# Performance work log

Measured on AMD Instinct MI355X. Metric: run time of the kernel, lower is better.

## Reference

```python
import jax, jax.numpy as jnp
import numpy as np

H = 256  # hidden_dim


def _bidir_lstm_layer(x, W_ih, W_hh, bias):
    """x: [S, B, in]; W_ih: [2, in, 4H]; W_hh: [2, H, 4H]; bias: [2, 4H].
    Returns [S, B, 2H] (forward || backward outputs per timestep).
    PyTorch gate order: i, f, g, o."""
    B = x.shape[1]
    init = (jnp.zeros((B, H), x.dtype), jnp.zeros((B, H), x.dtype))
    # precompute input projections for the whole sequence, both directions
    xp = jnp.einsum('sbi,dij->dsbj', x, W_ih) + bias[:, None, None, :]  # [2,S,B,4H]

    def make_step(W_hh_d):
        def step(carry, xt):
            h, c = carry
            g = xt + h @ W_hh_d  # [B, 4H]
            i = jax.nn.sigmoid(g[:, :H])
            f = jax.nn.sigmoid(g[:, H:2 * H])
            gg = jnp.tanh(g[:, 2 * H:3 * H])
            o = jax.nn.sigmoid(g[:, 3 * H:])
            c = f * c + i * gg
            h = o * jnp.tanh(c)
            return (h, c), h
        return step

    _, h_f = jax.lax.scan(make_step(W_hh[0]), init, xp[0])
    _, h_b = jax.lax.scan(make_step(W_hh[1]), init, xp[1], reverse=True)
    return jnp.concatenate([h_f, h_b], axis=-1)  # [S, B, 2H]


def setup_inputs() -> dict:
    key = jax.random.key(0)
    ks = jax.random.split(key, 11)
    s = 0.05  # small init scale to keep gates in their dynamic range
    inp = {
        'x': jax.random.normal(ks[0], (8192, 1024), jnp.float32),
        'w_ih0': jax.random.normal(ks[1], (2, 1024, 4 * H), jnp.float32) * s,
        'w_hh0': jax.random.normal(ks[2], (2, H, 4 * H), jnp.float32) * s,
        'b0': jax.random.normal(ks[3], (2, 4 * H), jnp.float32) * s,
        'w_ih': jax.random.normal(ks[4], (4, 2, 2 * H, 4 * H), jnp.float32) * s,
        'w_hh': jax.random.normal(ks[5], (4, 2, H, 4 * H), jnp.float32) * s,
        'b': jax.random.normal(ks[6], (4, 2, 4 * H), jnp.float32) * s,
        'w1': jax.random.normal(ks[7], (2 * H, 32), jnp.float32) * s,
        'b1': jax.random.normal(ks[8], (32,), jnp.float32) * s,
        'w2': jax.random.normal(ks[9], (32, 2), jnp.float32) * s,
        'b2': jax.random.normal(ks[10], (2,), jnp.float32) * s,
    }
    return inp


def reference(x, w_ih0, w_hh0, b0, w_ih, w_hh, b, w1, b1, w2, b2):
    # x: [S, 1024] -> [S, B=1, 1024] (module does unsqueeze(0).transpose(0,1))
    h = x[:, None, :]
    h = _bidir_lstm_layer(h, w_ih0, w_hh0, b0)
    for l in range(4):  # layers 1..4 (fixed count)
        h = _bidir_lstm_layer(h, w_ih[l], w_hh[l], b[l])
    # cat(forward output at last step, backward output at first step)
    feat = jnp.concatenate([h[-1, :, :H], h[0, :, H:]], axis=1)  # [1, 2H]
    out = (feat @ w1 + b1) @ w2 + b2  # [1, 2]
    return out
```

## Files before the change

### kernel.cpp

```cpp
#include <hip/hip_runtime.h>

constexpr int SQ = 8192;
constexpr int HD = 256;
constexpr int NG = 1024;

typedef __fp16 h2 __attribute__((ext_vector_type(2)));
typedef unsigned int uint;

__device__ __forceinline__ float sigm_f(float x) {
  float e = __builtin_amdgcn_exp2f(-1.4426950408889634f * x);
  return __builtin_amdgcn_rcpf(1.0f + e);
}
__device__ __forceinline__ float tanh_f(float x) {
  float e = __builtin_amdgcn_exp2f(2.885390081777927f * x);
  return 1.0f - 2.0f * __builtin_amdgcn_rcpf(1.0f + e);
}
__device__ __forceinline__ h2 bch2(uint v) { return __builtin_bit_cast(h2, v); }
__device__ __forceinline__ uint pk(float a, float b) {
  return __builtin_bit_cast(uint, __builtin_amdgcn_cvt_pkrtz(a, b));
}

__global__ __launch_bounds__(256) void gemm_xp(const float* __restrict__ A, int K,
                                               const float* __restrict__ W,
                                               const float* __restrict__ bias,
                                               float* __restrict__ out) {
  __shared__ float Al[16][64];
  __shared__ float Bl[16][64];
  const int tid = threadIdx.x;
  const int bm = blockIdx.x * 64;
  const int d  = blockIdx.y >> 4;
  const int bn = (blockIdx.y & 15) * 64;
  const float* Wd = W + (size_t)d * K * NG;
  const float* bd = bias + (size_t)d * NG;
  float* outd = out + (size_t)d * SQ * NG;

  const int m4 = (tid >> 4) << 2;
  const int n4 = (tid & 15) << 2;
  const int am = tid >> 2, ak = (tid & 3) << 2;
  const int bk = tid >> 4, bnn = (tid & 15) << 2;

  float acc[4][4] = {};
  for (int kt = 0; kt < K; kt += 16) {
    float4 av = *(const float4*)(A + (size_t)(bm + am) * K + kt + ak);
    float4 bv = *(const float4*)(Wd + (size_t)(kt + bk) * NG + bn + bnn);
    __syncthreads();
    Al[ak + 0][am] = av.x;
    Al[ak + 1][am] = av.y;
    Al[ak + 2][am] = av.z;
    Al[ak + 3][am] = av.w;
    *(float4*)&Bl[bk][bnn] = bv;
    __syncthreads();
#pragma unroll
    for (int k = 0; k < 16; ++k) {
      float4 a = *(const float4*)&Al[k][m4];
      float4 b = *(const float4*)&Bl[k][n4];
      float ar[4] = {a.x, a.y, a.z, a.w};
      float br[4] = {b.x, b.y, b.z, b.w};
#pragma unroll
      for (int i = 0; i < 4; ++i)
#pragma unroll
        for (int jj = 0; jj < 4; ++jj)
          acc[i][jj] = fmaf(ar[i], br[jj], acc[i][jj]);
    }
  }
#pragma unroll
  for (int i = 0; i < 4; ++i) {
    float4 o;
    o.x = acc[i][0] + bd[bn + n4 + 0];
    o.y = acc[i][1] + bd[bn + n4 + 1];
    o.z = acc[i][2] + bd[bn + n4 + 2];
    o.w = acc[i][3] + bd[bn + n4 + 3];
    *(float4*)(outd + (size_t)(bm + m4 + i) * NG + bn + n4) = o;
  }
}

__global__ __launch_bounds__(512, 1) void lstm_rec4(const float* __restrict__ Whh,
                                                    const float* __restrict__ xp,
                                                    float* __restrict__ obuf) {
  __shared__ uint4 wl4[8 * 1024];
  __shared__ float glds[1024];
  __shared__ uint4 hlds[32];
  const int d = blockIdx.x;
  const int j = threadIdx.x;
  const int w = j >> 6;
  const int l = j & 63;
  const int li = l & 31;
  const int s  = l >> 5;
  const float* W   = Whh + (size_t)d * HD * NG;
  const float* xpd = xp + (size_t)d * SQ * NG;
  const int cbase = w * 128 + li;

  for (int idx = j; idx < 8 * 1024; idx += 512) {
    const int q8 = idx >> 10;
    const int c  = idx & 1023;
    const int ss = q8 >> 2, q = q8 & 3;
    const int r0 = ss * 128 + 96 + 8 * q;
    uint4 v;
    v.x = pk(W[(size_t)(r0 + 0) * NG + c], W[(size_t)(r0 + 1) * NG + c]);
    v.y = pk(W[(size_t)(r0 + 2) * NG + c], W[(size_t)(r0 + 3) * NG + c]);
    v.z = pk(W[(size_t)(r0 + 4) * NG + c], W[(size_t)(r0 + 5) * NG + c]);
    v.w = pk(W[(size_t)(r0 + 6) * NG + c], W[(size_t)(r0 + 7) * NG + c]);
    wl4[q8 * 1024 + c] = v;
  }

  h2 wr[4][48];
#pragma unroll
  for (int i = 0; i < 4; ++i) {
    const float* Wc = W + (size_t)(s * 128) * NG + cbase + 32 * i;
#pragma unroll
    for (int k = 0; k < 48; ++k)
      wr[i][k] = __builtin_amdgcn_cvt_pkrtz(Wc[(size_t)(2 * k) * NG],
                                            Wc[(size_t)(2 * k + 1) * NG]);
  }

  if (j < 32) hlds[j] = make_uint4(0u, 0u, 0u, 0u);
  __syncthreads();

  const int fwd = (d == 0) ? 1 : 0;
  int t = fwd ? 0 : SQ - 1;
  const int dt = fwd ? 1 : -1;
  float cc = 0.0f;

  float xc[4] = {}, xn[4] = {};
  if (s == 0) {
#pragma unroll
    for (int i = 0; i < 4; ++i) xc[i] = xpd[(size_t)t * NG + cbase + 32 * i];
  }

  for (int step = 0; step < SQ; ++step) {
    if (s == 0 && step + 1 < SQ) {
#pragma unroll
      for (int i = 0; i < 4; ++i) xn[i] = xpd[(size_t)(t + dt) * NG + cbase + 32 * i];
    }

    float acc[4] = {0.0f, 0.0f, 0.0f, 0.0f};
    const uint4* hb = hlds + s * 16;

#pragma unroll
    for (int q = 0; q < 12; ++q) {
      uint4 hq = hb[q];
      h2 hx = bch2(hq.x), hy = bch2(hq.y), hz = bch2(hq.z), hw = bch2(hq.w);
#pragma unroll
      for (int i = 0; i < 4; ++i) {
        acc[i] = __builtin_amdgcn_fdot2(wr[i][4 * q + 0], hx, acc[i], false);
        acc[i] = __builtin_amdgcn_fdot2(wr[i][4 * q + 1], hy, acc[i], false);
        acc[i] = __builtin_amdgcn_fdot2(wr[i][4 * q + 2], hz, acc[i], false);
        acc[i] = __builtin_amdgcn_fdot2(wr[i][4 * q + 3], hw, acc[i], false);
      }
    }
#pragma unroll
    for (int qq = 0; qq < 4; ++qq) {
      uint4 hq = hb[12 + qq];
      h2 hx = bch2(hq.x), hy = bch2(hq.y), hz = bch2(hq.z), hw = bch2(hq.w);
#pragma unroll
      for (int i = 0; i < 4; ++i) {
        uint4 wq = wl4[(s * 4 + qq) * 1024 + cbase + 32 * i];
        acc[i] = __builtin_amdgcn_fdot2(bch2(wq.x), hx, acc[i], false);
        acc[i] = __builtin_amdgcn_fdot2(bch2(wq.y), hy, acc[i], false);
        acc[i] = __builtin_amdgcn_fdot2(bch2(wq.z), hz, acc[i], false);
        acc[i] = __builtin_amdgcn_fdot2(bch2(wq.w), hw, acc[i], false);
      }
    }

#pragma unroll
    for (int i = 0; i < 4; ++i) acc[i] += __shfl_xor(acc[i], 32);

    if (s == 0) {
#pragma unroll
      for (int i = 0; i < 4; ++i) {
        const int c = cbase + 32 * i;
        float pre = acc[i] + xc[i];
        float act = ((c >> 8) == 2) ? tanh_f(pre) : sigm_f(pre);
        glds[c] = act;
      }
    }
    __syncthreads();

    if (j < 256) {
      float iv = glds[j];
      float fv = glds[256 + j];
      float gv = glds[512 + j];
      float ov = glds[768 + j];
      cc = fv * cc + iv * gv;
      float hv = ov * tanh_f(cc);
      obuf[(size_t)t * 512 + (d << 8) + j] = hv;
      float hn = __shfl_down(hv, 1);
      if (!(j & 1))
        ((uint*)hlds)[j >> 1] = pk(hv, hn);
    }
    __syncthreads();

    if (s == 0) {
#pragma unroll
      for (int i = 0; i < 4; ++i) xc[i] = xn[i];
    }
    t += dt;
  }
}

__global__ void cls_k(const float* __restrict__ buf, const float* __restrict__ w1,
                      const float* __restrict__ b1, const float* __restrict__ w2,
                      const float* __restrict__ b2, float* __restrict__ out) {
  __shared__ float feat[512];
  __shared__ float hid[32];
  const int t = threadIdx.x;
  feat[t] = (t < 256) ? buf[(size_t)(SQ - 1) * 512 + t] : buf[t];
  __syncthreads();
  if (t < 32) {
    float a = b1[t];
    for (int k = 0; k < 512; ++k) a = fmaf(feat[k], w1[k * 32 + t], a);
    hid[t] = a;
  }
  __syncthreads();
  if (t < 2) {
    float a = b2[t];
    for (int k = 0; k < 32; ++k) a = fmaf(hid[k], w2[k * 2 + t], a);
    out[t] = a;
  }
}

extern "C" void kernel_launch(void* const* d_in, const int* in_sizes, int n_in,
                              void* d_out, int out_size, void* d_ws, size_t ws_size,
                              hipStream_t stream) {
  const float* x     = (const float*)d_in[0];
  const float* w_ih0 = (const float*)d_in[1];
  const float* w_hh0 = (const float*)d_in[2];
  const float* b0    = (const float*)d_in[3];
  const float* w_ih  = (const float*)d_in[4];
  const float* w_hh  = (const float*)d_in[5];
  const float* b     = (const float*)d_in[6];
  const float* w1    = (const float*)d_in[7];
  const float* b1    = (const float*)d_in[8];
  const float* w2    = (const float*)d_in[9];
  const float* b2    = (const float*)d_in[10];

  float* xp   = (float*)d_ws;
  float* bufA = xp + (size_t)2 * SQ * NG;
  float* bufB = bufA + (size_t)SQ * 512;

  const dim3 ggrid(SQ / 64, 32);

  gemm_xp<<<ggrid, 256, 0, stream>>>(x, 1024, w_ih0, b0, xp);
  lstm_rec4<<<2, 512, 0, stream>>>(w_hh0, xp, bufA);

  float* cur = bufA;
  float* nxt = bufB;
  for (int lyr = 0; lyr < 4; ++lyr) {
    gemm_xp<<<ggrid, 256, 0, stream>>>(cur, 512, w_ih + (size_t)lyr * 2 * 512 * 1024,
                                       b + (size_t)lyr * 2 * 1024, xp);
    lstm_rec4<<<2, 512, 0, stream>>>(w_hh + (size_t)lyr * 2 * 256 * 1024, xp, nxt);
    float* tmp = cur; cur = nxt; nxt = tmp;
  }

  cls_k<<<1, 512, 0, stream>>>(cur, w1, b1, w2, b2, (float*)d_out);
}
```

Measured before the change: 75.00 ms.

## Rework LSTM recurrence to 1024 threads with one barrier per step

The recurrence kernel now runs 1024 threads. Each thread holds its whole 64-row slice of W_hh in registers, so the weight slices previously kept in LDS are dropped. The four gates of a hidden unit are placed in the same lanes and reduced with two cross-lane shuffles, so the gate activations and cell update happen in-register without the glds exchange. A double-buffered, padded h buffer leaves one __syncthreads per timestep instead of two. The cost is one-wave-per-SIMD pressure, more shuffles, and only 16 of 64 lanes doing the elementwise update.

```diff
diff --git a/kernel.cpp b/kernel.cpp
--- a/kernel.cpp
+++ b/kernel.cpp
@@ -74,70 +74,54 @@
   }
 }
 
-__global__ __launch_bounds__(512, 1) void lstm_rec4(const float* __restrict__ Whh,
-                                                    const float* __restrict__ xp,
-                                                    float* __restrict__ obuf) {
-  __shared__ uint4 wl4[8 * 1024];
-  __shared__ float glds[1024];
-  __shared__ uint4 hlds[32];
+__global__ __launch_bounds__(1024, 1) void lstm_rec5(const float* __restrict__ Whh,
+                                                     const float* __restrict__ xp,
+                                                     float* __restrict__ obuf) {
+  __shared__ uint hldsd[2][144];
   const int d = blockIdx.x;
   const int j = threadIdx.x;
   const int w = j >> 6;
   const int l = j & 63;
-  const int li = l & 31;
-  const int s  = l >> 5;
+  const int u = w * 16 + (l & 15);
+  const int s = l >> 4;
   const float* W   = Whh + (size_t)d * HD * NG;
   const float* xpd = xp + (size_t)d * SQ * NG;
-  const int cbase = w * 128 + li;
-
-  for (int idx = j; idx < 8 * 1024; idx += 512) {
-    const int q8 = idx >> 10;
-    const int c  = idx & 1023;
-    const int ss = q8 >> 2, q = q8 & 3;
-    const int r0 = ss * 128 + 96 + 8 * q;
-    uint4 v;
-    v.x = pk(W[(size_t)(r0 + 0) * NG + c], W[(size_t)(r0 + 1) * NG + c]);
-    v.y = pk(W[(size_t)(r0 + 2) * NG + c], W[(size_t)(r0 + 3) * NG + c]);
-    v.z = pk(W[(size_t)(r0 + 4) * NG + c], W[(size_t)(r0 + 5) * NG + c]);
-    v.w = pk(W[(size_t)(r0 + 6) * NG + c], W[(size_t)(r0 + 7) * NG + c]);
-    wl4[q8 * 1024 + c] = v;
-  }
-
-  h2 wr[4][48];
+
+  h2 wr[4][32];
 #pragma unroll
   for (int i = 0; i < 4; ++i) {
-    const float* Wc = W + (size_t)(s * 128) * NG + cbase + 32 * i;
-#pragma unroll
-    for (int k = 0; k < 48; ++k)
+    const float* Wc = W + (size_t)(64 * s) * NG + u + 256 * i;
+#pragma unroll
+    for (int k = 0; k < 32; ++k)
       wr[i][k] = __builtin_amdgcn_cvt_pkrtz(Wc[(size_t)(2 * k) * NG],
                                             Wc[(size_t)(2 * k + 1) * NG]);
   }
 
-  if (j < 32) hlds[j] = make_uint4(0u, 0u, 0u, 0u);
+  if (j < 288) ((uint*)hldsd)[j] = 0u;
   __syncthreads();
 
   const int fwd = (d == 0) ? 1 : 0;
   int t = fwd ? 0 : SQ - 1;
   const int dt = fwd ? 1 : -1;
   float cc = 0.0f;
+  int p = 0;
 
   float xc[4] = {}, xn[4] = {};
-  if (s == 0) {
-#pragma unroll
-    for (int i = 0; i < 4; ++i) xc[i] = xpd[(size_t)t * NG + cbase + 32 * i];
+  if (l < 16) {
+#pragma unroll
+    for (int i = 0; i < 4; ++i) xc[i] = xpd[(size_t)t * NG + u + 256 * i];
   }
 
   for (int step = 0; step < SQ; ++step) {
-    if (s == 0 && step + 1 < SQ) {
-#pragma unroll
-      for (int i = 0; i < 4; ++i) xn[i] = xpd[(size_t)(t + dt) * NG + cbase + 32 * i];
-    }
-
+    if (l < 16 && step + 1 < SQ) {
+#pragma unroll
+      for (int i = 0; i < 4; ++i) xn[i] = xpd[(size_t)(t + dt) * NG + u + 256 * i];
+    }
+
+    const uint4* hb = (const uint4*)&hldsd[p][36 * s];
     float acc[4] = {0.0f, 0.0f, 0.0f, 0.0f};
-    const uint4* hb = hlds + s * 16;
-
-#pragma unroll
-    for (int q = 0; q < 12; ++q) {
+#pragma unroll
+    for (int q = 0; q < 8; ++q) {
       uint4 hq = hb[q];
       h2 hx = bch2(hq.x), hy = bch2(hq.y), hz = bch2(hq.z), hw = bch2(hq.w);
 #pragma unroll
@@ -148,52 +132,32 @@
         acc[i] = __builtin_amdgcn_fdot2(wr[i][4 * q + 3], hw, acc[i], false);
       }
     }
-#pragma unroll
-    for (int qq = 0; qq < 4; ++qq) {
-      uint4 hq = hb[12 + qq];
-      h2 hx = bch2(hq.x), hy = bch2(hq.y), hz = bch2(hq.z), hw = bch2(hq.w);
-#pragma unroll
-      for (int i = 0; i < 4; ++i) {
-        uint4 wq = wl4[(s * 4 + qq) * 1024 + cbase + 32 * i];
-        acc[i] = __builtin_amdgcn_fdot2(bch2(wq.x), hx, acc[i], false);
-        acc[i] = __builtin_amdgcn_fdot2(bch2(wq.y), hy, acc[i], false);
-        acc[i] = __builtin_amdgcn_fdot2(bch2(wq.z), hz, acc[i], false);
-        acc[i] = __builtin_amdgcn_fdot2(bch2(wq.w), hw, acc[i], false);
-      }
-    }
-
-#pragma unroll
-    for (int i = 0; i < 4; ++i) acc[i] += __shfl_xor(acc[i], 32);
-
-    if (s == 0) {
-#pragma unroll
-      for (int i = 0; i < 4; ++i) {
-        const int c = cbase + 32 * i;
-        float pre = acc[i] + xc[i];
-        float act = ((c >> 8) == 2) ? tanh_f(pre) : sigm_f(pre);
-        glds[c] = act;
-      }
-    }
-    __syncthreads();
-
-    if (j < 256) {
-      float iv = glds[j];
-      float fv = glds[256 + j];
-      float gv = glds[512 + j];
-      float ov = glds[768 + j];
+
+#pragma unroll
+    for (int i = 0; i < 4; ++i) {
+      acc[i] += __shfl_xor(acc[i], 16);
+      acc[i] += __shfl_xor(acc[i], 32);
+    }
+
+    if (l < 16) {
+      float iv = sigm_f(acc[0] + xc[0]);
+      float fv = sigm_f(acc[1] + xc[1]);
+      float gv = tanh_f(acc[2] + xc[2]);
+      float ov = sigm_f(acc[3] + xc[3]);
       cc = fv * cc + iv * gv;
       float hv = ov * tanh_f(cc);
-      obuf[(size_t)t * 512 + (d << 8) + j] = hv;
+      obuf[(size_t)t * 512 + (d << 8) + u] = hv;
       float hn = __shfl_down(hv, 1);
-      if (!(j & 1))
-        ((uint*)hlds)[j >> 1] = pk(hv, hn);
+      if (!(l & 1)) {
+        const int word = u >> 1;
+        hldsd[p ^ 1][36 * (word >> 5) + (word & 31)] = pk(hv, hn);
+      }
     }
     __syncthreads();
 
-    if (s == 0) {
-#pragma unroll
-      for (int i = 0; i < 4; ++i) xc[i] = xn[i];
-    }
+    p ^= 1;
+#pragma unroll
+    for (int i = 0; i < 4; ++i) xc[i] = xn[i];
     t += dt;
   }
 }
@@ -241,14 +205,14 @@
   const dim3 ggrid(SQ / 64, 32);
 
   gemm_xp<<<ggrid, 256, 0, stream>>>(x, 1024, w_ih0, b0, xp);
-  lstm_rec4<<<2, 512, 0, stream>>>(w_hh0, xp, bufA);
+  lstm_rec5<<<2, 1024, 0, stream>>>(w_hh0, xp, bufA);
 
   float* cur = bufA;
   float* nxt = bufB;
   for (int lyr = 0; lyr < 4; ++lyr) {
     gemm_xp<<<ggrid, 256, 0, stream>>>(cur, 512, w_ih + (size_t)lyr * 2 * 512 * 1024,
                                        b + (size_t)lyr * 2 * 1024, xp);
-    lstm_rec4<<<2, 512, 0, stream>>>(w_hh + (size_t)lyr * 2 * 256 * 1024, xp, nxt);
+    lstm_rec5<<<2, 1024, 0, stream>>>(w_hh + (size_t)lyr * 2 * 256 * 1024, xp, nxt);
     float* tmp = cur; cur = nxt; nxt = tmp;
   }
 
```

Result: slower. 153.4 ms (+104.5%).
